# Kernel optimization log

Hardware: AMD Instinct MI355X
Metric: run time of the kernel (lower is better)

Reference implementation:

```python
import jax, jax.numpy as jnp
import numpy as np

EMB = 1024
HEADS = 16
DK = EMB // HEADS
EPS = 1e-5


def setup_inputs() -> dict:
    key = jax.random.key(0)
    ks = jax.random.split(key, 7)
    s_in = 1.0 / np.sqrt(EMB)
    return {
        "x": jax.random.normal(ks[0], (4, 2048, EMB), dtype=jnp.float32),
        "W_qkv": jax.random.uniform(ks[1], (EMB, 3 * EMB), jnp.float32, -s_in, s_in),
        "b_qkv": jax.random.uniform(ks[2], (3 * EMB,), jnp.float32, -s_in, s_in),
        "W_out": jax.random.uniform(ks[3], (EMB, EMB), jnp.float32, -s_in, s_in),
        "b_out": jax.random.uniform(ks[4], (EMB,), jnp.float32, -s_in, s_in),
        "gamma": jnp.ones((EMB,), jnp.float32),
        "beta": jnp.zeros((EMB,), jnp.float32),
    }


def reference(x, W_qkv, b_qkv, W_out, b_out, gamma, beta):
    B, T, D = x.shape
    qkv = x @ W_qkv + b_qkv                      # [B,T,3D]
    q, k, v = jnp.split(qkv, 3, axis=-1)
    # [B,T,D] -> [B,H,T,dk]
    def heads(t):
        return t.reshape(B, T, HEADS, DK).transpose(0, 2, 1, 3)
    q, k, v = heads(q), heads(k), heads(v)
    scores = jnp.einsum("bhtd,bhsd->bhts", q, k) / np.sqrt(DK)
    attn = jax.nn.softmax(scores, axis=-1)
    out = jnp.einsum("bhts,bhsd->bhtd", attn, v)  # [B,H,T,dk]
    out = out.transpose(0, 2, 1, 3).reshape(B, T, D)
    out = out @ W_out + b_out
    res = x + out
    mu = jnp.mean(res, axis=-1, keepdims=True)
    var = jnp.mean((res - mu) ** 2, axis=-1, keepdims=True)
    return (res - mu) / jnp.sqrt(var + EPS) * gamma + beta
```

## Files before the change

### kernel.cpp

```cpp
#include <hip/hip_runtime.h>

#define B_ 4
#define T_ 2048
#define D_ 1024
#define H_ 16
#define DK_ 64
#define M_ (B_*T_)

typedef __bf16 bf16;
typedef __bf16 bf16x8 __attribute__((ext_vector_type(8)));
typedef __bf16 bf16x4 __attribute__((ext_vector_type(4)));
typedef short s16x4 __attribute__((ext_vector_type(4)));
typedef float f32x4 __attribute__((ext_vector_type(4)));

__device__ __forceinline__ f32x4 zero4() { f32x4 v = {0.f, 0.f, 0.f, 0.f}; return v; }

__device__ __forceinline__ float fexp2(float x) {
  float r;
  asm("v_exp_f32 %0, %1\n\ts_nop 0" : "=v"(r) : "v"(x));
  return r;
}

__device__ __forceinline__ float max3f(float a, float b, float c) {
  float r;
  asm("v_max3_f32 %0, %1, %2, %3" : "=v"(r) : "v"(a), "v"(b), "v"(c));
  return r;
}

__device__ __forceinline__ void g2l16(const void* g, void* l) {
  __builtin_amdgcn_global_load_lds(
      (const __attribute__((address_space(1))) void*)g,
      (__attribute__((address_space(3))) void*)l, 16, 0, 0);
}

__global__ __launch_bounds__(256) void cast_bf16(const float* __restrict__ src,
                                                 bf16* __restrict__ dst) {
  const size_t i = ((size_t)blockIdx.x * 256 + threadIdx.x) * 8;
  float4 a = *(const float4*)(src + i);
  float4 b = *(const float4*)(src + i + 4);
  bf16x8 v;
  v[0] = (bf16)a.x; v[1] = (bf16)a.y; v[2] = (bf16)a.z; v[3] = (bf16)a.w;
  v[4] = (bf16)b.x; v[5] = (bf16)b.y; v[6] = (bf16)b.z; v[7] = (bf16)b.w;
  *(bf16x8*)(dst + i) = v;
}

__global__ __launch_bounds__(256) void transpose_wf(const float* __restrict__ src,
                                                    bf16* __restrict__ dst, int R, int C) {
  __shared__ alignas(16) bf16 ts[64 * 65];
  const int tid = threadIdx.x;
  const int r0 = blockIdx.x * 64, c0 = blockIdx.y * 64;
  {
    int rr = tid >> 2, cc = (tid & 3) * 16;
    const float4* p4 = (const float4*)(src + (size_t)(r0 + rr) * C + c0 + cc);
    float fv[16];
#pragma unroll
    for (int q = 0; q < 4; ++q) *(float4*)&fv[q * 4] = p4[q];
#pragma unroll
    for (int i = 0; i < 16; ++i) ts[(cc + i) * 65 + rr] = (bf16)fv[i];
  }
  __syncthreads();
  {
    int rr = tid >> 2, cc = (tid & 3) * 16;
    bf16x8 a, b;
#pragma unroll
    for (int i = 0; i < 8; ++i) a[i] = ts[rr * 65 + cc + i];
#pragma unroll
    for (int i = 0; i < 8; ++i) b[i] = ts[rr * 65 + cc + 8 + i];
    bf16* q = dst + (size_t)(c0 + rr) * R + r0 + cc;
    *(bf16x8*)q = a;
    *(bf16x8*)(q + 8) = b;
  }
}

__global__ __launch_bounds__(256) void transpose_v(const bf16* __restrict__ qkv,
                                                   bf16* __restrict__ Vt) {
  __shared__ alignas(16) bf16 ts[64 * 65];
  int bid = blockIdx.x;
  const int tt = bid & 31; bid >>= 5;
  const int h = bid & 15;  const int b = bid >> 4;
  const int t0 = tt * 64;
  const int tid = threadIdx.x;
  {
    int tok = tid >> 2, fc = (tid & 3) * 16;
    const bf16* p = qkv + (size_t)(b * T_ + t0 + tok) * (3 * D_) + 2 * D_ + h * DK_ + fc;
    bf16x8 a = *(const bf16x8*)p;
    bf16x8 c = *(const bf16x8*)(p + 8);
#pragma unroll
    for (int i = 0; i < 8; ++i) ts[(fc + i) * 65 + tok] = a[i];
#pragma unroll
    for (int i = 0; i < 8; ++i) ts[(fc + 8 + i) * 65 + tok] = c[i];
  }
  __syncthreads();
  {
    int f = tid >> 2, tc = (tid & 3) * 16;
    bf16x8 a, c;
#pragma unroll
    for (int i = 0; i < 8; ++i) a[i] = ts[f * 65 + tc + i];
#pragma unroll
    for (int i = 0; i < 8; ++i) c[i] = ts[f * 65 + tc + 8 + i];
    bf16* q = Vt + ((size_t)(b * H_ + h) * DK_ + f) * T_ + t0 + tc;
    *(bf16x8*)q = a;
    *(bf16x8*)(q + 8) = c;
  }
}

template <int ASRC, bool FUSE>
__global__ __launch_bounds__(256) void gemm128(const void* __restrict__ Av,
                                               const bf16* __restrict__ Bt,
                                               const float* __restrict__ bias,
                                               bf16* __restrict__ Cbf,
                                               float* __restrict__ Cf,
                                               const float* __restrict__ resid,
                                               int N, int K, int lda, int ldc) {
  __shared__ alignas(16) bf16 As[128 * 32];
  __shared__ alignas(16) bf16 Bs[128 * 32];
  const int tid = threadIdx.x;
  const int wid = tid >> 6, lane = tid & 63, quad = lane >> 4, l16 = lane & 15;
  const int m0 = blockIdx.x * 128, n0 = blockIdx.y * 128;
  const int wr = (wid >> 1) * 64, wc = (wid & 1) * 64;

  f32x4 acc[4][4];
#pragma unroll
  for (int i = 0; i < 4; ++i)
#pragma unroll
    for (int j = 0; j < 4; ++j) acc[i][j] = zero4();

  for (int k0 = 0; k0 < K; k0 += 32) {
    bf16x8 ar[2];
    if (ASRC == 0) {
#pragma unroll
      for (int p = 0; p < 2; ++p) {
        int t = p * 256 + tid;
        int row = t >> 2, kc = (t & 3) * 8;
        const float* ap = (const float*)Av + (size_t)(m0 + row) * lda + k0 + kc;
        float4 a0 = *(const float4*)ap, a1 = *(const float4*)(ap + 4);
        bf16x8 v;
        v[0] = (bf16)a0.x; v[1] = (bf16)a0.y; v[2] = (bf16)a0.z; v[3] = (bf16)a0.w;
        v[4] = (bf16)a1.x; v[5] = (bf16)a1.y; v[6] = (bf16)a1.z; v[7] = (bf16)a1.w;
        ar[p] = v;
      }
    }
    __syncthreads();
#pragma unroll
    for (int p = 0; p < 2; ++p) {
      int t = p * 256 + tid;
      int row = t >> 2, kc = (t & 3) * 8;
      g2l16(Bt + (size_t)(n0 + row) * K + k0 + kc, (char*)Bs + p * 4096 + wid * 1024);
      if (ASRC == 1)
        g2l16((const bf16*)Av + (size_t)(m0 + row) * lda + k0 + kc,
              (char*)As + p * 4096 + wid * 1024);
      else
        *(bf16x8*)&As[row * 32 + kc] = ar[p];
    }
    __syncthreads();
    bf16x8 af[4], bfr[4];
#pragma unroll
    for (int i = 0; i < 4; ++i)
      af[i] = *(const bf16x8*)&As[(wr + i * 16 + l16) * 32 + quad * 8];
#pragma unroll
    for (int j = 0; j < 4; ++j)
      bfr[j] = *(const bf16x8*)&Bs[(wc + j * 16 + l16) * 32 + quad * 8];
#pragma unroll
    for (int i = 0; i < 4; ++i)
#pragma unroll
      for (int j = 0; j < 4; ++j)
        acc[i][j] = __builtin_amdgcn_mfma_f32_16x16x32_bf16(af[i], bfr[j], acc[i][j], 0, 0, 0);
  }

#pragma unroll
  for (int i = 0; i < 4; ++i) {
#pragma unroll
    for (int j = 0; j < 4; ++j) {
      const int col = n0 + wc + j * 16 + l16;
      const float bv = bias[col];
#pragma unroll
      for (int r = 0; r < 4; ++r) {
        const int row = m0 + wr + i * 16 + quad * 4 + r;
        const float v = acc[i][j][r] + bv;
        if (FUSE) {
          const size_t off = (size_t)row * N + col;
          Cf[off] = v + resid[off];
        } else {
          Cbf[(size_t)row * ldc + col] = (bf16)v;
        }
      }
    }
  }
}

__global__ __launch_bounds__(512, 2) void attn256(const bf16* __restrict__ qkv,
                                                  const bf16* __restrict__ Vt,
                                                  bf16* __restrict__ out) {
  __shared__ alignas(16) bf16 Ks[128 * 72];
  __shared__ alignas(16) bf16 Vs[64 * 136];
  const int tid = threadIdx.x;
  const int wid = tid >> 6, lane = tid & 63, quad = lane >> 4, l16 = lane & 15;
  const int bid = blockIdx.x;
  const int qb = bid & 7, h = (bid >> 3) & 15, b = bid >> 7;
  const int q0 = qb * 256;

  const int skey = tid >> 3, sf = (tid & 7) * 8;
  const int svf = tid >> 4, skc = (tid & 15) * 8;
  const bf16* kbase = qkv + (size_t)(b * T_ + skey) * (3 * D_) + D_ + h * DK_ + sf;
  const bf16* vbase = Vt + ((size_t)(b * H_ + h) * DK_ + svf) * T_ + skc;

  const float SC = 0.125f * 1.44269504f;
  bf16x8 qA[2], qB[2];
  {
    const bf16* qpA = qkv + (size_t)(b * T_ + q0 + wid * 32 + l16) * (3 * D_) + h * DK_ + quad * 8;
    const bf16* qpB = qpA + (size_t)16 * (3 * D_);
    qA[0] = *(const bf16x8*)qpA;       qA[1] = *(const bf16x8*)(qpA + 32);
    qB[0] = *(const bf16x8*)qpB;       qB[1] = *(const bf16x8*)(qpB + 32);
#pragma unroll
    for (int i = 0; i < 8; ++i) {
      qA[0][i] = (bf16)((float)qA[0][i] * SC); qA[1][i] = (bf16)((float)qA[1][i] * SC);
      qB[0][i] = (bf16)((float)qB[0][i] * SC); qB[1][i] = (bf16)((float)qB[1][i] * SC);
    }
  }

  float miA = -1e30f, liA = 0.f, miB = -1e30f, liB = 0.f;
  f32x4 oA[4], oB[4];
#pragma unroll
  for (int ft = 0; ft < 4; ++ft) { oA[ft] = zero4(); oB[ft] = zero4(); }

  bf16x8 kr[2], vr[2];
#pragma unroll
  for (int p = 0; p < 2; ++p) {
    kr[p] = *(const bf16x8*)(kbase + (size_t)(p * 64) * (3 * D_));
    vr[p] = *(const bf16x8*)(vbase + (size_t)(p * 32) * T_);
  }

  for (int kt = 0; kt < T_ / 128; ++kt) {
    __syncthreads();
#pragma unroll
    for (int p = 0; p < 2; ++p) {
      *(bf16x8*)&Ks[(skey + p * 64) * 72 + sf] = kr[p];
      *(bf16x8*)&Vs[(svf + p * 32) * 136 + skc] = vr[p];
    }
    __syncthreads();
    if (kt + 1 < T_ / 128) {
      const size_t koff = (size_t)(kt + 1) * 128;
#pragma unroll
      for (int p = 0; p < 2; ++p) {
        kr[p] = *(const bf16x8*)(kbase + (koff + p * 64) * (3 * D_));
        vr[p] = *(const bf16x8*)(vbase + (size_t)(p * 32) * T_ + koff);
      }
    }

    f32x4 svA[8], svB[8];
#pragma unroll
    for (int nt = 0; nt < 8; ++nt) { svA[nt] = zero4(); svB[nt] = zero4(); }
    __builtin_amdgcn_s_setprio(1);
#pragma unroll
    for (int nt = 0; nt < 8; ++nt)
#pragma unroll
      for (int ks = 0; ks < 2; ++ks) {
        bf16x8 kf = *(const bf16x8*)&Ks[(nt * 16 + l16) * 72 + ks * 32 + quad * 8];
        svA[nt] = __builtin_amdgcn_mfma_f32_16x16x32_bf16(kf, qA[ks], svA[nt], 0, 0, 0);
        svB[nt] = __builtin_amdgcn_mfma_f32_16x16x32_bf16(kf, qB[ks], svB[nt], 0, 0, 0);
      }
    __builtin_amdgcn_s_setprio(0);

    float a0 = max3f(svA[0][0], svA[0][1], svA[0][2]);
    float a1 = max3f(svA[0][3], svA[1][0], svA[1][1]);
    a0 = max3f(a0, svA[1][2], svA[1][3]);
    float b0 = max3f(svB[0][0], svB[0][1], svB[0][2]);
    float b1 = max3f(svB[0][3], svB[1][0], svB[1][1]);
    b0 = max3f(b0, svB[1][2], svB[1][3]);
#pragma unroll
    for (int nt = 2; nt < 8; nt += 2) {
      a0 = max3f(a0, svA[nt][0], svA[nt][1]);
      a1 = max3f(a1, svA[nt][2], svA[nt][3]);
      a0 = max3f(a0, svA[nt + 1][0], svA[nt + 1][1]);
      a1 = max3f(a1, svA[nt + 1][2], svA[nt + 1][3]);
      b0 = max3f(b0, svB[nt][0], svB[nt][1]);
      b1 = max3f(b1, svB[nt][2], svB[nt][3]);
      b0 = max3f(b0, svB[nt + 1][0], svB[nt + 1][1]);
      b1 = max3f(b1, svB[nt + 1][2], svB[nt + 1][3]);
    }
    float tA = fmaxf(a0, a1), tB = fmaxf(b0, b1);
    tA = fmaxf(tA, __shfl_xor(tA, 16, 64));
    tA = fmaxf(tA, __shfl_xor(tA, 32, 64));
    tB = fmaxf(tB, __shfl_xor(tB, 16, 64));
    tB = fmaxf(tB, __shfl_xor(tB, 32, 64));

    if (!__all(tA <= miA + 8.f)) {
      const float nm = fmaxf(miA, tA);
      const float al = fexp2(miA - nm);
      miA = nm; liA *= al;
#pragma unroll
      for (int r = 0; r < 4; ++r) {
        const float ar = __shfl(al, quad * 4 + r, 64);
#pragma unroll
        for (int ft = 0; ft < 4; ++ft) oA[ft][r] *= ar;
      }
    }
    if (!__all(tB <= miB + 8.f)) {
      const float nm = fmaxf(miB, tB);
      const float al = fexp2(miB - nm);
      miB = nm; liB *= al;
#pragma unroll
      for (int r = 0; r < 4; ++r) {
        const float ar = __shfl(al, quad * 4 + r, 64);
#pragma unroll
        for (int ft = 0; ft < 4; ++ft) oB[ft][r] *= ar;
      }
    }

    s16x4 pA[8], pB[8];
    f32x4 s4A = zero4(), s4B = zero4();
#pragma unroll
    for (int nt = 0; nt < 8; ++nt) {
      f32x4 dA = svA[nt] - miA;
      dA[0] = fexp2(dA[0]); dA[1] = fexp2(dA[1]); dA[2] = fexp2(dA[2]); dA[3] = fexp2(dA[3]);
      s4A += dA;
      union { bf16x4 b; s16x4 s; } ua;
#pragma unroll
      for (int j = 0; j < 4; ++j) ua.b[j] = (bf16)dA[j];
      pA[nt] = ua.s;
      f32x4 dB = svB[nt] - miB;
      dB[0] = fexp2(dB[0]); dB[1] = fexp2(dB[1]); dB[2] = fexp2(dB[2]); dB[3] = fexp2(dB[3]);
      s4B += dB;
      union { bf16x4 b; s16x4 s; } ub;
#pragma unroll
      for (int j = 0; j < 4; ++j) ub.b[j] = (bf16)dB[j];
      pB[nt] = ub.s;
    }
    float sA = (s4A[0] + s4A[1]) + (s4A[2] + s4A[3]);
    float sB = (s4B[0] + s4B[1]) + (s4B[2] + s4B[3]);
    sA += __shfl_xor(sA, 16, 64);
    sA += __shfl_xor(sA, 32, 64);
    sB += __shfl_xor(sB, 16, 64);
    sB += __shfl_xor(sB, 32, 64);
    liA += sA; liB += sB;

    __builtin_amdgcn_s_setprio(1);
#pragma unroll
    for (int ks = 0; ks < 8; ++ks)
#pragma unroll
      for (int ft = 0; ft < 4; ++ft) {
        const s16x4 vf = *(const s16x4*)&Vs[(ft * 16 + l16) * 136 + ks * 16 + quad * 4];
        oA[ft] = __builtin_amdgcn_mfma_f32_16x16x16bf16_1k(pA[ks], vf, oA[ft], 0, 0, 0);
        oB[ft] = __builtin_amdgcn_mfma_f32_16x16x16bf16_1k(pB[ks], vf, oB[ft], 0, 0, 0);
      }
    __builtin_amdgcn_s_setprio(0);
  }

#pragma unroll
  for (int r = 0; r < 4; ++r) {
    const float invA = 1.0f / __shfl(liA, quad * 4 + r, 64);
    const float invB = 1.0f / __shfl(liB, quad * 4 + r, 64);
    const int rowA = b * T_ + q0 + wid * 32 + quad * 4 + r;
    const int rowB = rowA + 16;
#pragma unroll
    for (int ft = 0; ft < 4; ++ft) {
      out[(size_t)rowA * (3 * D_) + h * DK_ + ft * 16 + l16] = (bf16)(oA[ft][r] * invA);
      out[(size_t)rowB * (3 * D_) + h * DK_ + ft * 16 + l16] = (bf16)(oB[ft][r] * invB);
    }
  }
}

__global__ __launch_bounds__(256) void ln_out(float* __restrict__ res,
                                              const float* __restrict__ gamma,
                                              const float* __restrict__ beta) {
  const int row = blockIdx.x * 4 + (threadIdx.x >> 6);
  const int lane = threadIdx.x & 63;
  float4 v[4];
  float s = 0.f, q = 0.f;
#pragma unroll
  for (int p = 0; p < 4; ++p) {
    v[p] = *(const float4*)(res + (size_t)row * D_ + p * 256 + lane * 4);
    s += v[p].x + v[p].y + v[p].z + v[p].w;
    q += v[p].x * v[p].x + v[p].y * v[p].y + v[p].z * v[p].z + v[p].w * v[p].w;
  }
#pragma unroll
  for (int m = 1; m < 64; m <<= 1) { s += __shfl_xor(s, m, 64); q += __shfl_xor(q, m, 64); }
  const float mu = s * (1.0f / D_);
  const float var = q * (1.0f / D_) - mu * mu;
  const float rstd = rsqrtf(var + 1e-5f);
#pragma unroll
  for (int p = 0; p < 4; ++p) {
    const int c = p * 256 + lane * 4;
    const float4 g = *(const float4*)(gamma + c);
    const float4 be = *(const float4*)(beta + c);
    float4 ov;
    ov.x = (v[p].x - mu) * rstd * g.x + be.x;
    ov.y = (v[p].y - mu) * rstd * g.y + be.y;
    ov.z = (v[p].z - mu) * rstd * g.z + be.z;
    ov.w = (v[p].w - mu) * rstd * g.w + be.w;
    *(float4*)(res + (size_t)row * D_ + c) = ov;
  }
}

extern "C" void kernel_launch(void* const* d_in, const int* in_sizes, int n_in,
                              void* d_out, int out_size, void* d_ws, size_t ws_size,
                              hipStream_t stream) {
  const float* x     = (const float*)d_in[0];
  const float* Wqkv  = (const float*)d_in[1];
  const float* bqkv  = (const float*)d_in[2];
  const float* Wout  = (const float*)d_in[3];
  const float* bout  = (const float*)d_in[4];
  const float* gamma = (const float*)d_in[5];
  const float* beta  = (const float*)d_in[6];
  float* out = (float*)d_out;

  char* ws = (char*)d_ws;
  bf16* WqkvT = (bf16*)ws; ws += (size_t)3 * D_ * D_ * 2;
  bf16* WoutT = (bf16*)ws; ws += (size_t)D_ * D_ * 2;
  bf16* qkv   = (bf16*)ws; ws += (size_t)M_ * 3 * D_ * 2;
  bf16* Vt    = (bf16*)ws;
  bf16* attn  = qkv + 2 * D_;
  bf16* xb    = Vt;

  transpose_wf<<<dim3(D_ / 64, 3 * D_ / 64), 256, 0, stream>>>(Wqkv, WqkvT, D_, 3 * D_);
  transpose_wf<<<dim3(D_ / 64, D_ / 64), 256, 0, stream>>>(Wout, WoutT, D_, D_);
  cast_bf16<<<M_ * D_ / (256 * 8), 256, 0, stream>>>(x, xb);
  gemm128<1, false><<<dim3(M_ / 128, 3 * D_ / 128), 256, 0, stream>>>(
      xb, WqkvT, bqkv, qkv, nullptr, nullptr, 3 * D_, D_, D_, 3 * D_);
  transpose_v<<<B_ * H_ * (T_ / 64), 256, 0, stream>>>(qkv, Vt);
  attn256<<<B_ * H_ * (T_ / 256), 512, 0, stream>>>(qkv, Vt, attn);
  gemm128<1, true><<<dim3(M_ / 128, D_ / 128), 256, 0, stream>>>(
      attn, WoutT, bout, nullptr, out, x, D_, D_, 3 * D_, D_);
  ln_out<<<M_ / 4, 256, 0, stream>>>(out, gamma, beta);
}
```

Before: 333.2 us.

## Double-buffer attention K/V tiles with direct global-to-LDS loads and XOR swizzle

```diff
diff --git a/kernel.cpp b/kernel.cpp
--- a/kernel.cpp
+++ b/kernel.cpp
@@ -188,21 +188,21 @@
   }
 }
 
-__global__ __launch_bounds__(512, 2) void attn256(const bf16* __restrict__ qkv,
+__global__ __launch_bounds__(256, 4) void attn_db(const bf16* __restrict__ qkv,
                                                   const bf16* __restrict__ Vt,
                                                   bf16* __restrict__ out) {
-  __shared__ alignas(16) bf16 Ks[128 * 72];
-  __shared__ alignas(16) bf16 Vs[64 * 136];
+  __shared__ alignas(16) bf16 Ks[2][64 * 64];
+  __shared__ alignas(16) bf16 Vs[2][64 * 64];
   const int tid = threadIdx.x;
   const int wid = tid >> 6, lane = tid & 63, quad = lane >> 4, l16 = lane & 15;
   const int bid = blockIdx.x;
-  const int qb = bid & 7, h = (bid >> 3) & 15, b = bid >> 7;
-  const int q0 = qb * 256;
-
-  const int skey = tid >> 3, sf = (tid & 7) * 8;
-  const int svf = tid >> 4, skc = (tid & 15) * 8;
-  const bf16* kbase = qkv + (size_t)(b * T_ + skey) * (3 * D_) + D_ + h * DK_ + sf;
-  const bf16* vbase = Vt + ((size_t)(b * H_ + h) * DK_ + svf) * T_ + skc;
+  const int qb = bid & 15, h = (bid >> 4) & 15, b = bid >> 8;
+  const int q0 = qb * 128;
+
+  const int lrow8 = lane >> 3;
+  const int kch = (lane & 7) ^ lrow8;
+  const bf16* kg = qkv + (size_t)(b * T_ + wid * 16 + lrow8) * (3 * D_) + D_ + h * DK_ + kch * 8;
+  const bf16* vg = Vt + ((size_t)(b * H_ + h) * DK_ + wid * 16 + lrow8) * T_ + kch * 8;
 
   const float SC = 0.125f * 1.44269504f;
   bf16x8 qA[2], qB[2];
@@ -223,39 +223,30 @@
 #pragma unroll
   for (int ft = 0; ft < 4; ++ft) { oA[ft] = zero4(); oB[ft] = zero4(); }
 
-  bf16x8 kr[2], vr[2];
-#pragma unroll
-  for (int p = 0; p < 2; ++p) {
-    kr[p] = *(const bf16x8*)(kbase + (size_t)(p * 64) * (3 * D_));
-    vr[p] = *(const bf16x8*)(vbase + (size_t)(p * 32) * T_);
-  }
-
-  for (int kt = 0; kt < T_ / 128; ++kt) {
-    __syncthreads();
-#pragma unroll
-    for (int p = 0; p < 2; ++p) {
-      *(bf16x8*)&Ks[(skey + p * 64) * 72 + sf] = kr[p];
-      *(bf16x8*)&Vs[(svf + p * 32) * 136 + skc] = vr[p];
-    }
-    __syncthreads();
-    if (kt + 1 < T_ / 128) {
-      const size_t koff = (size_t)(kt + 1) * 128;
-#pragma unroll
-      for (int p = 0; p < 2; ++p) {
-        kr[p] = *(const bf16x8*)(kbase + (koff + p * 64) * (3 * D_));
-        vr[p] = *(const bf16x8*)(vbase + (size_t)(p * 32) * T_ + koff);
-      }
-    }
-
-    f32x4 svA[8], svB[8];
-#pragma unroll
-    for (int nt = 0; nt < 8; ++nt) { svA[nt] = zero4(); svB[nt] = zero4(); }
+  auto stage = [&](int buf, int t0) {
+    g2l16(kg + (size_t)(t0 + 0) * (3 * D_), &Ks[buf][(wid * 16 + 0) * 64]);
+    g2l16(kg + (size_t)(t0 + 8) * (3 * D_), &Ks[buf][(wid * 16 + 8) * 64]);
+    g2l16(vg + (size_t)0 * T_ + t0,         &Vs[buf][(wid * 16 + 0) * 64]);
+    g2l16(vg + (size_t)8 * T_ + t0,         &Vs[buf][(wid * 16 + 8) * 64]);
+  };
+
+  stage(0, 0);
+  __syncthreads();
+
+  for (int kt = 0; kt < T_ / 64; ++kt) {
+    const int cur = kt & 1;
+    if (kt + 1 < T_ / 64) stage(cur ^ 1, (kt + 1) * 64);
+
+    f32x4 svA[4], svB[4];
+#pragma unroll
+    for (int nt = 0; nt < 4; ++nt) { svA[nt] = zero4(); svB[nt] = zero4(); }
     __builtin_amdgcn_s_setprio(1);
 #pragma unroll
-    for (int nt = 0; nt < 8; ++nt)
+    for (int nt = 0; nt < 4; ++nt)
 #pragma unroll
       for (int ks = 0; ks < 2; ++ks) {
-        bf16x8 kf = *(const bf16x8*)&Ks[(nt * 16 + l16) * 72 + ks * 32 + quad * 8];
+        const bf16x8 kf = *(const bf16x8*)
+            &Ks[cur][(nt * 16 + l16) * 64 + (((ks << 2) | quad) ^ (l16 & 7)) * 8];
         svA[nt] = __builtin_amdgcn_mfma_f32_16x16x32_bf16(kf, qA[ks], svA[nt], 0, 0, 0);
         svB[nt] = __builtin_amdgcn_mfma_f32_16x16x32_bf16(kf, qB[ks], svB[nt], 0, 0, 0);
       }
@@ -264,20 +255,17 @@
     float a0 = max3f(svA[0][0], svA[0][1], svA[0][2]);
     float a1 = max3f(svA[0][3], svA[1][0], svA[1][1]);
     a0 = max3f(a0, svA[1][2], svA[1][3]);
+    a1 = max3f(a1, svA[2][0], svA[2][1]);
+    a0 = max3f(a0, svA[2][2], svA[2][3]);
+    a1 = max3f(a1, svA[3][0], svA[3][1]);
+    a0 = max3f(a0, svA[3][2], svA[3][3]);
     float b0 = max3f(svB[0][0], svB[0][1], svB[0][2]);
     float b1 = max3f(svB[0][3], svB[1][0], svB[1][1]);
     b0 = max3f(b0, svB[1][2], svB[1][3]);
-#pragma unroll
-    for (int nt = 2; nt < 8; nt += 2) {
-      a0 = max3f(a0, svA[nt][0], svA[nt][1]);
-      a1 = max3f(a1, svA[nt][2], svA[nt][3]);
-      a0 = max3f(a0, svA[nt + 1][0], svA[nt + 1][1]);
-      a1 = max3f(a1, svA[nt + 1][2], svA[nt + 1][3]);
-      b0 = max3f(b0, svB[nt][0], svB[nt][1]);
-      b1 = max3f(b1, svB[nt][2], svB[nt][3]);
-      b0 = max3f(b0, svB[nt + 1][0], svB[nt + 1][1]);
-      b1 = max3f(b1, svB[nt + 1][2], svB[nt + 1][3]);
-    }
+    b1 = max3f(b1, svB[2][0], svB[2][1]);
+    b0 = max3f(b0, svB[2][2], svB[2][3]);
+    b1 = max3f(b1, svB[3][0], svB[3][1]);
+    b0 = max3f(b0, svB[3][2], svB[3][3]);
     float tA = fmaxf(a0, a1), tB = fmaxf(b0, b1);
     tA = fmaxf(tA, __shfl_xor(tA, 16, 64));
     tA = fmaxf(tA, __shfl_xor(tA, 32, 64));
@@ -307,10 +295,10 @@
       }
     }
 
-    s16x4 pA[8], pB[8];
+    s16x4 pA[4], pB[4];
     f32x4 s4A = zero4(), s4B = zero4();
 #pragma unroll
-    for (int nt = 0; nt < 8; ++nt) {
+    for (int nt = 0; nt < 4; ++nt) {
       f32x4 dA = svA[nt] - miA;
       dA[0] = fexp2(dA[0]); dA[1] = fexp2(dA[1]); dA[2] = fexp2(dA[2]); dA[3] = fexp2(dA[3]);
       s4A += dA;
@@ -336,14 +324,18 @@
 
     __builtin_amdgcn_s_setprio(1);
 #pragma unroll
-    for (int ks = 0; ks < 8; ++ks)
+    for (int ks = 0; ks < 4; ++ks)
 #pragma unroll
       for (int ft = 0; ft < 4; ++ft) {
-        const s16x4 vf = *(const s16x4*)&Vs[(ft * 16 + l16) * 136 + ks * 16 + quad * 4];
+        const s16x4 vf = *(const s16x4*)
+            &Vs[cur][(ft * 16 + l16) * 64 +
+                     ((ks * 2 + (quad >> 1)) ^ (l16 & 7)) * 8 + (quad & 1) * 4];
         oA[ft] = __builtin_amdgcn_mfma_f32_16x16x16bf16_1k(pA[ks], vf, oA[ft], 0, 0, 0);
         oB[ft] = __builtin_amdgcn_mfma_f32_16x16x16bf16_1k(pB[ks], vf, oB[ft], 0, 0, 0);
       }
     __builtin_amdgcn_s_setprio(0);
+
+    __syncthreads();
   }
 
 #pragma unroll
@@ -418,7 +410,7 @@
   gemm128<1, false><<<dim3(M_ / 128, 3 * D_ / 128), 256, 0, stream>>>(
       xb, WqkvT, bqkv, qkv, nullptr, nullptr, 3 * D_, D_, D_, 3 * D_);
   transpose_v<<<B_ * H_ * (T_ / 64), 256, 0, stream>>>(qkv, Vt);
-  attn256<<<B_ * H_ * (T_ / 256), 512, 0, stream>>>(qkv, Vt, attn);
+  attn_db<<<B_ * H_ * (T_ / 128), 256, 0, stream>>>(qkv, Vt, attn);
   gemm128<1, true><<<dim3(M_ / 128, D_ / 128), 256, 0, stream>>>(
       attn, WoutT, bout, nullptr, out, x, D_, D_, 3 * D_, D_);
   ln_out<<<M_ / 4, 256, 0, stream>>>(out, gamma, beta);
```

Result: no change. 330.5 us (-0.8%).
